# Performance work log

Measured on AMD Instinct MI355X. Metric: run time of the kernel, lower is better.

The kernel has to match this reference:

```python
import jax, jax.numpy as jnp
import numpy as np

B, S, D_IN, D_OUT = 4, 4096, 1024, 64

def setup_inputs() -> dict:
    key = jax.random.key(0)
    ks = jax.random.split(key, 7)
    return {
        "x":  jax.random.normal(ks[0], (B, S, D_IN), dtype=jnp.float32),
        "Wq": jax.random.normal(ks[1], (D_IN, D_OUT), dtype=jnp.float32) * 0.02,
        "bq": jax.random.normal(ks[2], (D_OUT,), dtype=jnp.float32) * 0.02,
        "Wk": jax.random.normal(ks[3], (D_IN, D_OUT), dtype=jnp.float32) * 0.02,
        "bk": jax.random.normal(ks[4], (D_OUT,), dtype=jnp.float32) * 0.02,
        "Wv": jax.random.normal(ks[5], (D_IN, D_OUT), dtype=jnp.float32) * 0.02,
        "bv": jax.random.normal(ks[6], (D_OUT,), dtype=jnp.float32) * 0.02,
    }

def reference(x, Wq, bq, Wk, bk, Wv, bv):
    # x: [B, S, d_in]
    seq = x.shape[1]
    q = x @ Wq + bq            # [B, S, d_out]
    k = x @ Wk + bk
    v = x @ Wv + bv
    scores = jnp.einsum("bqd,bkd->bqk", q, k)          # [B, S, S]
    causal = jnp.triu(jnp.ones((seq, seq), dtype=bool), k=1)
    scores = jnp.where(causal[None, :, :], -jnp.inf, scores)
    # NOTE: original code scales by sqrt(token_len), not sqrt(d_out) (d_k = keys.shape[1])
    scale = jnp.sqrt(jnp.asarray(seq, dtype=scores.dtype))
    attn = jax.nn.softmax(scores / scale, axis=-1)      # [B, S, S]
    # dropout in the original is applied but its result is discarded -> no-op
    return jnp.einsum("bqk,bkd->bqd", attn, v)          # [B, S, d_out]
```

## Files before the change

kernel.cpp:

```cpp
#include <hip/hip_runtime.h>
#include <math.h>

#define B 4
#define S 4096
#define DIN 1024
#define DOUT 64
#define BS (B * S)

typedef __bf16 bf16;
typedef __bf16 bf16x4 __attribute__((ext_vector_type(4)));
typedef __bf16 bf16x8 __attribute__((ext_vector_type(8)));
typedef float f32x4 __attribute__((ext_vector_type(4)));

#define QSCALE 0.022542110013890053f

#define QS_OFF 0
#define KF_OFF (2u * 1024 * 1024)
#define VF_OFF (4u * 1024 * 1024)
#define WP_OFF (6u * 1024 * 1024)
#define OP_OFF (7u * 1024 * 1024)
#define LP_OFF (23u * 1024 * 1024)

__global__ __launch_bounds__(256) void wpack_kernel(
    const float* __restrict__ Wq, const float* __restrict__ Wk,
    const float* __restrict__ Wv, bf16* __restrict__ wp) {
  const int t = blockIdx.x * 256 + threadIdx.x;
  const int m = t >> 16;
  const int r = t & 65535;
  const int k = r >> 6;
  const int n64 = r & 63;
  const float* W = (m == 0) ? Wq : (m == 1) ? Wk : Wv;
  const float v = W[r];
  const int n = m * 64 + n64;
  const int nt = n >> 4;
  const int lane = ((k >> 3) & 3) * 16 + (n & 15);
  const int idx = ((nt * 32 + (k >> 5)) * 64 + lane) * 8 + (k & 7);
  wp[idx] = (bf16)v;
}

__global__ __launch_bounds__(256) void qkv_mfma_kernel(
    const float* __restrict__ x, const float* __restrict__ bq,
    const float* __restrict__ bk, const float* __restrict__ bv,
    const bf16* __restrict__ wp, bf16* __restrict__ Qs,
    bf16* __restrict__ KF, bf16* __restrict__ VF) {
  __shared__ __align__(16) bf16 xt[32][520];

  const int tid = threadIdx.x;
  const int wid = tid >> 6;
  const int lane = tid & 63;
  const int l15 = lane & 15;
  const int quad = lane >> 4;
  const int blk = blockIdx.x;

  const bf16x8* wp8 = (const bf16x8*)wp;

  f32x4 acc[3][2];
#pragma unroll
  for (int j = 0; j < 3; ++j)
#pragma unroll
    for (int st = 0; st < 2; ++st) acc[j][st] = (f32x4)(0.f);

  for (int ph = 0; ph < 2; ++ph) {
    if (ph) __syncthreads();
    {
      float4 v[16];
#pragma unroll
      for (int i = 0; i < 16; ++i) {
        const int ch = i * 256 + tid;
        const int row = ch >> 7;
        const int col4 = ch & 127;
        v[i] = *(const float4*)(x + (size_t)(blk * 32 + row) * DIN + ph * 512 +
                                col4 * 4);
      }
#pragma unroll
      for (int i = 0; i < 16; ++i) {
        const int ch = i * 256 + tid;
        const int row = ch >> 7;
        const int col4 = ch & 127;
        bf16x4 c;
        c[0] = (bf16)v[i].x; c[1] = (bf16)v[i].y;
        c[2] = (bf16)v[i].z; c[3] = (bf16)v[i].w;
        *(bf16x4*)&xt[row][col4 * 4] = c;
      }
    }
    __syncthreads();

#pragma unroll 4
    for (int kc = 0; kc < 16; ++kc) {
      bf16x8 bfr[3];
#pragma unroll
      for (int j = 0; j < 3; ++j)
        bfr[j] = wp8[((wid * 3 + j) * 32 + ph * 16 + kc) * 64 + lane];
      const bf16x8 a0 = *(const bf16x8*)&xt[l15][quad * 8 + kc * 32];
      const bf16x8 a1 = *(const bf16x8*)&xt[16 + l15][quad * 8 + kc * 32];
#pragma unroll
      for (int j = 0; j < 3; ++j) {
        acc[j][0] = __builtin_amdgcn_mfma_f32_16x16x32_bf16(a0, bfr[j], acc[j][0], 0, 0, 0);
        acc[j][1] = __builtin_amdgcn_mfma_f32_16x16x32_bf16(a1, bfr[j], acc[j][1], 0, 0, 0);
      }
    }
  }

#pragma unroll
  for (int j = 0; j < 3; ++j) {
    const int nt = wid * 3 + j;
    const int sel = nt >> 2;
    const int c = (nt & 3) * 16 + l15;
    const float bias = ((sel == 0) ? bq : (sel == 1) ? bk : bv)[c];
#pragma unroll
    for (int st = 0; st < 2; ++st) {
      const int row0 = blk * 32 + st * 16 + quad * 4;
      if (sel == 0) {
#pragma unroll
        for (int r = 0; r < 4; ++r)
          Qs[(size_t)(row0 + r) * DOUT + c] =
              (bf16)((acc[j][st][r] + bias) * QSCALE);
      } else if (sel == 1) {
        const size_t kb =
            ((size_t)(((row0 >> 6) * 4 + ((row0 >> 4) & 3)) * 2 + (c >> 5)) * 64 +
             ((c >> 3) & 3) * 16 + quad * 4) * 8 + (c & 7);
#pragma unroll
        for (int r = 0; r < 4; ++r)
          KF[kb + r * 8] = (bf16)(acc[j][st][r] + bias);
      } else {
        const size_t vb =
            ((size_t)(((row0 >> 6) * 2 + ((row0 >> 5) & 1)) * 4 + (c >> 4)) * 64 +
             (c & 15) + 16 * ((row0 >> 3) & 3)) * 8 + (row0 & 7);
        bf16x4 vv;
#pragma unroll
        for (int r = 0; r < 4; ++r) vv[r] = (bf16)(acc[j][st][r] + bias);
        *(bf16x4*)(VF + vb) = vv;
      }
    }
  }
}

__global__ __launch_bounds__(256) void attn_mfma_kernel(
    const bf16* __restrict__ Qs, const bf16* __restrict__ KFp,
    const bf16* __restrict__ VFp, bf16* __restrict__ Oh,
    float* __restrict__ lh) {
  __shared__ __align__(16) bf16 pw[4][32][72];

  const int tid = threadIdx.x;
  const int wid = tid >> 6;
  const int lane = tid & 63;
  const int l15 = lane & 15;
  const int quad = lane >> 4;
  const int b = blockIdx.x & 3;
  const int half = (blockIdx.x >> 2) & 1;
  const int s32 = 127 - (blockIdx.x >> 3);
  const int ntiles = (s32 >> 1) + 1;
  const int e = half * 4 + wid;
  const int t0 = (e * ntiles) >> 3;
  const int t1 = ((e + 1) * ntiles) >> 3;

  const bf16x8* KF8 = (const bf16x8*)KFp;
  const bf16x8* VF8 = (const bf16x8*)VFp;
  const int tb0 = b * 64;

  const bf16* Qb = Qs + ((size_t)b * S + s32 * 32) * DOUT;
  bf16x8 qf[2][2];
#pragma unroll
  for (int st = 0; st < 2; ++st)
#pragma unroll
    for (int k = 0; k < 2; ++k)
      qf[st][k] =
          *(const bf16x8*)(Qb + (st * 16 + l15) * DOUT + k * 32 + quad * 8);

  f32x4 o[2][4];
#pragma unroll
  for (int st = 0; st < 2; ++st)
#pragma unroll
    for (int i = 0; i < 4; ++i) o[st][i] = (f32x4)(0.f);
  f32x4 lsum[2] = {(f32x4)(0.f), (f32x4)(0.f)};

  for (int t = t0; t < t1; ++t) {
    const int tb = tb0 + t;
    bf16x8 kf[8], vf[8];
#pragma unroll
    for (int nt = 0; nt < 4; ++nt)
#pragma unroll
      for (int c = 0; c < 2; ++c)
        kf[nt * 2 + c] = KF8[(size_t)((tb * 4 + nt) * 2 + c) * 64 + lane];
#pragma unroll
    for (int c = 0; c < 2; ++c)
#pragma unroll
      for (int ntd = 0; ntd < 4; ++ntd)
        vf[c * 4 + ntd] = VF8[(size_t)((tb * 2 + c) * 4 + ntd) * 64 + lane];

    f32x4 s[2][4];
#pragma unroll
    for (int st = 0; st < 2; ++st)
#pragma unroll
      for (int nt = 0; nt < 4; ++nt) {
        s[st][nt] = __builtin_amdgcn_mfma_f32_16x16x32_bf16(
            qf[st][0], kf[nt * 2 + 0], (f32x4)(0.f), 0, 0, 0);
        s[st][nt] = __builtin_amdgcn_mfma_f32_16x16x32_bf16(
            qf[st][1], kf[nt * 2 + 1], s[st][nt], 0, 0, 0);
      }

    if (t == ntiles - 1) {
#pragma unroll
      for (int st = 0; st < 2; ++st)
#pragma unroll
        for (int nt = 0; nt < 4; ++nt) {
          const int key = t * 64 + nt * 16 + l15;
#pragma unroll
          for (int r = 0; r < 4; ++r) {
            const int qrow = s32 * 32 + st * 16 + quad * 4 + r;
            const float p = (key <= qrow) ? exp2f(fminf(s[st][nt][r], 44.f)) : 0.f;
            lsum[st][r] += p;
            pw[wid][st * 16 + quad * 4 + r][nt * 16 + l15] = (bf16)p;
          }
        }
    } else {
#pragma unroll
      for (int st = 0; st < 2; ++st)
#pragma unroll
        for (int nt = 0; nt < 4; ++nt)
#pragma unroll
          for (int r = 0; r < 4; ++r) {
            const float p = exp2f(fminf(s[st][nt][r], 44.f));
            lsum[st][r] += p;
            pw[wid][st * 16 + quad * 4 + r][nt * 16 + l15] = (bf16)p;
          }
    }

#pragma unroll
    for (int st = 0; st < 2; ++st) {
      const bf16x8 pf0 = *(const bf16x8*)&pw[wid][st * 16 + l15][quad * 8];
      const bf16x8 pf1 = *(const bf16x8*)&pw[wid][st * 16 + l15][32 + quad * 8];
#pragma unroll
      for (int ntd = 0; ntd < 4; ++ntd) {
        o[st][ntd] = __builtin_amdgcn_mfma_f32_16x16x32_bf16(
            pf0, vf[0 * 4 + ntd], o[st][ntd], 0, 0, 0);
        o[st][ntd] = __builtin_amdgcn_mfma_f32_16x16x32_bf16(
            pf1, vf[1 * 4 + ntd], o[st][ntd], 0, 0, 0);
      }
    }
  }

#pragma unroll
  for (int m = 1; m < 16; m <<= 1)
#pragma unroll
    for (int st = 0; st < 2; ++st)
#pragma unroll
      for (int r = 0; r < 4; ++r) lsum[st][r] += __shfl_xor(lsum[st][r], m, 64);

  const int slot = (b * 128 + s32) * 8 + e;
  if (l15 == 0) {
#pragma unroll
    for (int st = 0; st < 2; ++st)
#pragma unroll
      for (int r = 0; r < 4; ++r)
        lh[slot * 32 + st * 16 + quad * 4 + r] = lsum[st][r];
  }
#pragma unroll
  for (int st = 0; st < 2; ++st)
#pragma unroll
    for (int ntd = 0; ntd < 4; ++ntd)
#pragma unroll
      for (int r = 0; r < 4; ++r)
        Oh[(size_t)slot * 2048 + (st * 16 + quad * 4 + r) * 64 + ntd * 16 + l15] =
            (bf16)o[st][ntd][r];
}

__global__ __launch_bounds__(256) void combine_kernel(
    const bf16* __restrict__ Oh, const float* __restrict__ lh,
    float* __restrict__ out) {
  const int gid = blockIdx.x * 256 + threadIdx.x;
  const int token = gid >> 4;
  const int d4 = (gid & 15) * 4;
  const int b = token >> 12;
  const int s = token & 4095;
  const int s32 = s >> 5;
  const int qq = s & 31;
  const int slot0 = (b * 128 + s32) * 8;
  f32x4 acc = (f32x4)(0.f);
  float l = 0.f;
#pragma unroll
  for (int q = 0; q < 8; ++q) {
    const bf16x4 ov =
        *(const bf16x4*)(Oh + (size_t)(slot0 + q) * 2048 + qq * 64 + d4);
#pragma unroll
    for (int i = 0; i < 4; ++i) acc[i] += (float)ov[i];
    l += lh[(slot0 + q) * 32 + qq];
  }
  ((f32x4*)out)[gid] = acc * (1.f / l);
}

extern "C" void kernel_launch(void* const* d_in, const int* in_sizes, int n_in,
                              void* d_out, int out_size, void* d_ws,
                              size_t ws_size, hipStream_t stream) {
  const float* x  = (const float*)d_in[0];
  const float* Wq = (const float*)d_in[1];
  const float* bq = (const float*)d_in[2];
  const float* Wk = (const float*)d_in[3];
  const float* bk = (const float*)d_in[4];
  const float* Wv = (const float*)d_in[5];
  const float* bv = (const float*)d_in[6];
  float* out = (float*)d_out;

  char* ws = (char*)d_ws;
  bf16* Qs = (bf16*)(ws + QS_OFF);
  bf16* KF = (bf16*)(ws + KF_OFF);
  bf16* VF = (bf16*)(ws + VF_OFF);
  bf16* wp = (bf16*)(ws + WP_OFF);
  bf16* Oh = (bf16*)(ws + OP_OFF);
  float* lh = (float*)(ws + LP_OFF);

  wpack_kernel<<<768, 256, 0, stream>>>(Wq, Wk, Wv, wp);
  qkv_mfma_kernel<<<512, 256, 0, stream>>>(x, bq, bk, bv, wp, Qs, KF, VF);
  attn_mfma_kernel<<<1024, 256, 0, stream>>>(Qs, KF, VF, Oh, lh);
  combine_kernel<<<1024, 256, 0, stream>>>(Oh, lh, out);
}
```

Baseline: 150.4 us.

## Double waves in QKV projection and prefetch second x half during first MMA phase

The QKV projection block goes from 256 to 512 threads, with each wave handling one 16-row subtile instead of two, so there are more waves to hide latency. The global load of the second half of x is issued before the first-phase MFMA loop and written to shared memory afterwards, overlapping load latency with compute. The trade-off is that every wave now reloads the same weight fragments, doubling weight traffic per block, and the prefetched values occupy extra registers.

```diff
diff --git a/kernel.cpp b/kernel.cpp
--- a/kernel.cpp
+++ b/kernel.cpp
@@ -38,7 +38,7 @@
   wp[idx] = (bf16)v;
 }
 
-__global__ __launch_bounds__(256) void qkv_mfma_kernel(
+__global__ __launch_bounds__(512, 4) void qkv_mfma_kernel(
     const float* __restrict__ x, const float* __restrict__ bq,
     const float* __restrict__ bk, const float* __restrict__ bv,
     const bf16* __restrict__ wp, bf16* __restrict__ Qs,
@@ -50,87 +50,104 @@
   const int lane = tid & 63;
   const int l15 = lane & 15;
   const int quad = lane >> 4;
+  const int st = wid >> 2;
+  const int w4 = wid & 3;
   const int blk = blockIdx.x;
 
   const bf16x8* wp8 = (const bf16x8*)wp;
 
-  f32x4 acc[3][2];
-#pragma unroll
-  for (int j = 0; j < 3; ++j)
-#pragma unroll
-    for (int st = 0; st < 2; ++st) acc[j][st] = (f32x4)(0.f);
-
-  for (int ph = 0; ph < 2; ++ph) {
-    if (ph) __syncthreads();
-    {
-      float4 v[16];
-#pragma unroll
-      for (int i = 0; i < 16; ++i) {
-        const int ch = i * 256 + tid;
-        const int row = ch >> 7;
-        const int col4 = ch & 127;
-        v[i] = *(const float4*)(x + (size_t)(blk * 32 + row) * DIN + ph * 512 +
-                                col4 * 4);
-      }
-#pragma unroll
-      for (int i = 0; i < 16; ++i) {
-        const int ch = i * 256 + tid;
-        const int row = ch >> 7;
-        const int col4 = ch & 127;
-        bf16x4 c;
-        c[0] = (bf16)v[i].x; c[1] = (bf16)v[i].y;
-        c[2] = (bf16)v[i].z; c[3] = (bf16)v[i].w;
-        *(bf16x4*)&xt[row][col4 * 4] = c;
-      }
-    }
-    __syncthreads();
+  f32x4 acc[3];
+#pragma unroll
+  for (int j = 0; j < 3; ++j) acc[j] = (f32x4)(0.f);
+
+  float4 v[8];
+
+#pragma unroll
+  for (int i = 0; i < 8; ++i) {
+    const int ch = i * 512 + tid;
+    v[i] = *(const float4*)(x + (size_t)(blk * 32 + (ch >> 7)) * DIN +
+                            (ch & 127) * 4);
+  }
+#pragma unroll
+  for (int i = 0; i < 8; ++i) {
+    const int ch = i * 512 + tid;
+    bf16x4 c4;
+    c4[0] = (bf16)v[i].x; c4[1] = (bf16)v[i].y;
+    c4[2] = (bf16)v[i].z; c4[3] = (bf16)v[i].w;
+    *(bf16x4*)&xt[ch >> 7][(ch & 127) * 4] = c4;
+  }
+  __syncthreads();
+
+#pragma unroll
+  for (int i = 0; i < 8; ++i) {
+    const int ch = i * 512 + tid;
+    v[i] = *(const float4*)(x + (size_t)(blk * 32 + (ch >> 7)) * DIN + 512 +
+                            (ch & 127) * 4);
+  }
+  __builtin_amdgcn_sched_barrier(0);
 
 #pragma unroll 4
-    for (int kc = 0; kc < 16; ++kc) {
-      bf16x8 bfr[3];
-#pragma unroll
-      for (int j = 0; j < 3; ++j)
-        bfr[j] = wp8[((wid * 3 + j) * 32 + ph * 16 + kc) * 64 + lane];
-      const bf16x8 a0 = *(const bf16x8*)&xt[l15][quad * 8 + kc * 32];
-      const bf16x8 a1 = *(const bf16x8*)&xt[16 + l15][quad * 8 + kc * 32];
-#pragma unroll
-      for (int j = 0; j < 3; ++j) {
-        acc[j][0] = __builtin_amdgcn_mfma_f32_16x16x32_bf16(a0, bfr[j], acc[j][0], 0, 0, 0);
-        acc[j][1] = __builtin_amdgcn_mfma_f32_16x16x32_bf16(a1, bfr[j], acc[j][1], 0, 0, 0);
-      }
-    }
+  for (int kc = 0; kc < 16; ++kc) {
+    bf16x8 bfr[3];
+#pragma unroll
+    for (int j = 0; j < 3; ++j)
+      bfr[j] = wp8[((w4 * 3 + j) * 32 + kc) * 64 + lane];
+    const bf16x8 a = *(const bf16x8*)&xt[st * 16 + l15][quad * 8 + kc * 32];
+#pragma unroll
+    for (int j = 0; j < 3; ++j)
+      acc[j] = __builtin_amdgcn_mfma_f32_16x16x32_bf16(a, bfr[j], acc[j], 0, 0, 0);
+  }
+  __syncthreads();
+
+#pragma unroll
+  for (int i = 0; i < 8; ++i) {
+    const int ch = i * 512 + tid;
+    bf16x4 c4;
+    c4[0] = (bf16)v[i].x; c4[1] = (bf16)v[i].y;
+    c4[2] = (bf16)v[i].z; c4[3] = (bf16)v[i].w;
+    *(bf16x4*)&xt[ch >> 7][(ch & 127) * 4] = c4;
+  }
+  __syncthreads();
+
+#pragma unroll 4
+  for (int kc = 0; kc < 16; ++kc) {
+    bf16x8 bfr[3];
+#pragma unroll
+    for (int j = 0; j < 3; ++j)
+      bfr[j] = wp8[((w4 * 3 + j) * 32 + 16 + kc) * 64 + lane];
+    const bf16x8 a = *(const bf16x8*)&xt[st * 16 + l15][quad * 8 + kc * 32];
+#pragma unroll
+    for (int j = 0; j < 3; ++j)
+      acc[j] = __builtin_amdgcn_mfma_f32_16x16x32_bf16(a, bfr[j], acc[j], 0, 0, 0);
   }
 
 #pragma unroll
   for (int j = 0; j < 3; ++j) {
-    const int nt = wid * 3 + j;
+    const int nt = w4 * 3 + j;
     const int sel = nt >> 2;
     const int c = (nt & 3) * 16 + l15;
     const float bias = ((sel == 0) ? bq : (sel == 1) ? bk : bv)[c];
-#pragma unroll
-    for (int st = 0; st < 2; ++st) {
-      const int row0 = blk * 32 + st * 16 + quad * 4;
-      if (sel == 0) {
-#pragma unroll
-        for (int r = 0; r < 4; ++r)
-          Qs[(size_t)(row0 + r) * DOUT + c] =
-              (bf16)((acc[j][st][r] + bias) * QSCALE);
-      } else if (sel == 1) {
-        const size_t kb =
-            ((size_t)(((row0 >> 6) * 4 + ((row0 >> 4) & 3)) * 2 + (c >> 5)) * 64 +
-             ((c >> 3) & 3) * 16 + quad * 4) * 8 + (c & 7);
-#pragma unroll
-        for (int r = 0; r < 4; ++r)
-          KF[kb + r * 8] = (bf16)(acc[j][st][r] + bias);
-      } else {
-        const size_t vb =
-            ((size_t)(((row0 >> 6) * 2 + ((row0 >> 5) & 1)) * 4 + (c >> 4)) * 64 +
-             (c & 15) + 16 * ((row0 >> 3) & 3)) * 8 + (row0 & 7);
-        bf16x4 vv;
-#pragma unroll
-        for (int r = 0; r < 4; ++r) vv[r] = (bf16)(acc[j][st][r] + bias);
-        *(bf16x4*)(VF + vb) = vv;
-      }
+    const int row0 = blk * 32 + st * 16 + quad * 4;
+    if (sel == 0) {
+#pragma unroll
+      for (int r = 0; r < 4; ++r)
+        Qs[(size_t)(row0 + r) * DOUT + c] =
+            (bf16)((acc[j][r] + bias) * QSCALE);
+    } else if (sel == 1) {
+      const size_t kb =
+          ((size_t)(((row0 >> 6) * 4 + ((row0 >> 4) & 3)) * 2 + (c >> 5)) * 64 +
+           ((c >> 3) & 3) * 16 + quad * 4) * 8 + (c & 7);
+#pragma unroll
+      for (int r = 0; r < 4; ++r)
+        KF[kb + r * 8] = (bf16)(acc[j][r] + bias);
+    } else {
+      const size_t vb =
+          ((size_t)(((row0 >> 6) * 2 + ((row0 >> 5) & 1)) * 4 + (c >> 4)) * 64 +
+           (c & 15) + 16 * ((row0 >> 3) & 3)) * 8 + (row0 & 7);
+      bf16x4 vv;
+#pragma unroll
+      for (int r = 0; r < 4; ++r) vv[r] = (bf16)(acc[j][r] + bias);
+      *(bf16x4*)(VF + vb) = vv;
     }
   }
 }
@@ -310,7 +327,7 @@
   float* lh = (float*)(ws + LP_OFF);
 
   wpack_kernel<<<768, 256, 0, stream>>>(Wq, Wk, Wv, wp);
-  qkv_mfma_kernel<<<512, 256, 0, stream>>>(x, bq, bk, bv, wp, Qs, KF, VF);
+  qkv_mfma_kernel<<<512, 512, 0, stream>>>(x, bq, bk, bv, wp, Qs, KF, VF);
   attn_mfma_kernel<<<1024, 256, 0, stream>>>(Qs, KF, VF, Oh, lh);
   combine_kernel<<<1024, 256, 0, stream>>>(Oh, lh, out);
 }
```

Measured after the change: 151.7 us. Within noise of the previous version (+0.9%).

## Fuse QKV projection and attention into one persistent kernel with per-batch counters

Applied to the files above, without the earlier changes.

Merges the QKV projection and attention kernels into a single 512-block launch. Each block first computes its projection tile, then signals a per-batch atomic counter, and then runs two attention work units after spinning until every projection block of that batch has finished. The counters are zeroed in the weight-pack kernel. This removes a kernel launch and lets attention for one batch start while other batches are still projecting. In exchange it relies on all 512 blocks being co-resident (launch bounds request 2 blocks per CU) to avoid deadlock, and adds spin-wait and fence overhead.

```diff
diff --git a/kernel.cpp b/kernel.cpp
--- a/kernel.cpp
+++ b/kernel.cpp
@@ -20,10 +20,13 @@
 #define WP_OFF (6u * 1024 * 1024)
 #define OP_OFF (7u * 1024 * 1024)
 #define LP_OFF (23u * 1024 * 1024)
+#define CNT_OFF (30u * 1024 * 1024)
 
 __global__ __launch_bounds__(256) void wpack_kernel(
     const float* __restrict__ Wq, const float* __restrict__ Wk,
-    const float* __restrict__ Wv, bf16* __restrict__ wp) {
+    const float* __restrict__ Wv, bf16* __restrict__ wp,
+    int* __restrict__ cnt) {
+  if (blockIdx.x == 0 && threadIdx.x < 4) cnt[threadIdx.x] = 0;
   const int t = blockIdx.x * 256 + threadIdx.x;
   const int m = t >> 16;
   const int r = t & 65535;
@@ -38,231 +41,248 @@
   wp[idx] = (bf16)v;
 }
 
-__global__ __launch_bounds__(256) void qkv_mfma_kernel(
+__global__ __launch_bounds__(256, 2) void qkvattn_kernel(
     const float* __restrict__ x, const float* __restrict__ bq,
     const float* __restrict__ bk, const float* __restrict__ bv,
     const bf16* __restrict__ wp, bf16* __restrict__ Qs,
-    bf16* __restrict__ KF, bf16* __restrict__ VF) {
-  __shared__ __align__(16) bf16 xt[32][520];
+    bf16* __restrict__ KF, bf16* __restrict__ VF, bf16* __restrict__ Oh,
+    float* __restrict__ lh, int* __restrict__ cnt) {
+  __shared__ __align__(16) char smem[33280];
 
   const int tid = threadIdx.x;
+  const int bid = blockIdx.x;
   const int wid = tid >> 6;
   const int lane = tid & 63;
   const int l15 = lane & 15;
   const int quad = lane >> 4;
-  const int blk = blockIdx.x;
-
-  const bf16x8* wp8 = (const bf16x8*)wp;
-
-  f32x4 acc[3][2];
-#pragma unroll
-  for (int j = 0; j < 3; ++j)
-#pragma unroll
-    for (int st = 0; st < 2; ++st) acc[j][st] = (f32x4)(0.f);
-
-  for (int ph = 0; ph < 2; ++ph) {
-    if (ph) __syncthreads();
-    {
-      float4 v[16];
-#pragma unroll
-      for (int i = 0; i < 16; ++i) {
-        const int ch = i * 256 + tid;
-        const int row = ch >> 7;
-        const int col4 = ch & 127;
-        v[i] = *(const float4*)(x + (size_t)(blk * 32 + row) * DIN + ph * 512 +
-                                col4 * 4);
-      }
-#pragma unroll
-      for (int i = 0; i < 16; ++i) {
-        const int ch = i * 256 + tid;
-        const int row = ch >> 7;
-        const int col4 = ch & 127;
-        bf16x4 c;
-        c[0] = (bf16)v[i].x; c[1] = (bf16)v[i].y;
-        c[2] = (bf16)v[i].z; c[3] = (bf16)v[i].w;
-        *(bf16x4*)&xt[row][col4 * 4] = c;
-      }
+
+  {
+    bf16(*xt)[520] = (bf16(*)[520])smem;
+    const int blk = bid;
+    const bf16x8* wp8 = (const bf16x8*)wp;
+
+    f32x4 acc[3][2];
+#pragma unroll
+    for (int j = 0; j < 3; ++j)
+#pragma unroll
+      for (int st = 0; st < 2; ++st) acc[j][st] = (f32x4)(0.f);
+
+    for (int ph = 0; ph < 2; ++ph) {
+      if (ph) __syncthreads();
+      {
+        float4 v[16];
+#pragma unroll
+        for (int i = 0; i < 16; ++i) {
+          const int ch = i * 256 + tid;
+          const int row = ch >> 7;
+          const int col4 = ch & 127;
+          v[i] = *(const float4*)(x + (size_t)(blk * 32 + row) * DIN +
+                                  ph * 512 + col4 * 4);
+        }
+#pragma unroll
+        for (int i = 0; i < 16; ++i) {
+          const int ch = i * 256 + tid;
+          const int row = ch >> 7;
+          const int col4 = ch & 127;
+          bf16x4 c;
+          c[0] = (bf16)v[i].x; c[1] = (bf16)v[i].y;
+          c[2] = (bf16)v[i].z; c[3] = (bf16)v[i].w;
+          *(bf16x4*)&xt[row][col4 * 4] = c;
+        }
+      }
+      __syncthreads();
+
+#pragma unroll 4
+      for (int kc = 0; kc < 16; ++kc) {
+        bf16x8 bfr[3];
+#pragma unroll
+        for (int j = 0; j < 3; ++j)
+          bfr[j] = wp8[((wid * 3 + j) * 32 + ph * 16 + kc) * 64 + lane];
+        const bf16x8 a0 = *(const bf16x8*)&xt[l15][quad * 8 + kc * 32];
+        const bf16x8 a1 = *(const bf16x8*)&xt[16 + l15][quad * 8 + kc * 32];
+#pragma unroll
+        for (int j = 0; j < 3; ++j) {
+          acc[j][0] = __builtin_amdgcn_mfma_f32_16x16x32_bf16(a0, bfr[j],
+                                                              acc[j][0], 0, 0, 0);
+          acc[j][1] = __builtin_amdgcn_mfma_f32_16x16x32_bf16(a1, bfr[j],
+                                                              acc[j][1], 0, 0, 0);
+        }
+      }
+    }
+
+#pragma unroll
+    for (int j = 0; j < 3; ++j) {
+      const int nt = wid * 3 + j;
+      const int sel = nt >> 2;
+      const int c = (nt & 3) * 16 + l15;
+      const float bias = ((sel == 0) ? bq : (sel == 1) ? bk : bv)[c];
+#pragma unroll
+      for (int st = 0; st < 2; ++st) {
+        const int row0 = blk * 32 + st * 16 + quad * 4;
+        if (sel == 0) {
+#pragma unroll
+          for (int r = 0; r < 4; ++r)
+            Qs[(size_t)(row0 + r) * DOUT + c] =
+                (bf16)((acc[j][st][r] + bias) * QSCALE);
+        } else if (sel == 1) {
+          const size_t kb =
+              ((size_t)(((row0 >> 6) * 4 + ((row0 >> 4) & 3)) * 2 + (c >> 5)) *
+                   64 + ((c >> 3) & 3) * 16 + quad * 4) * 8 + (c & 7);
+#pragma unroll
+          for (int r = 0; r < 4; ++r)
+            KF[kb + r * 8] = (bf16)(acc[j][st][r] + bias);
+        } else {
+          const size_t vb =
+              ((size_t)(((row0 >> 6) * 2 + ((row0 >> 5) & 1)) * 4 + (c >> 4)) *
+                   64 + (c & 15) + 16 * ((row0 >> 3) & 3)) * 8 + (row0 & 7);
+          bf16x4 vv;
+#pragma unroll
+          for (int r = 0; r < 4; ++r) vv[r] = (bf16)(acc[j][st][r] + bias);
+          *(bf16x4*)(VF + vb) = vv;
+        }
+      }
+    }
+  }
+
+  __threadfence();
+  __syncthreads();
+  if (tid == 0)
+    __hip_atomic_fetch_add(&cnt[bid >> 7], 1, __ATOMIC_RELEASE,
+                           __HIP_MEMORY_SCOPE_AGENT);
+
+  bf16(*pw)[32][72] = (bf16(*)[32][72])smem;
+  const bf16x8* KF8 = (const bf16x8*)KF;
+  const bf16x8* VF8 = (const bf16x8*)VF;
+
+#pragma unroll 1
+  for (int pass = 0; pass < 2; ++pass) {
+    const int u = pass ? (512 + (bid ^ 128)) : bid;
+    const int b = u >> 8;
+    const int rr = u & 255;
+    const int s32 = 127 - (rr >> 1);
+    const int half = rr & 1;
+    const int ntiles = (s32 >> 1) + 1;
+    const int e = half * 4 + wid;
+    const int t0 = (e * ntiles) >> 3;
+    const int t1 = ((e + 1) * ntiles) >> 3;
+    const int tb0 = b * 64;
+
+    if (tid == 0) {
+      while (__hip_atomic_load(&cnt[b], __ATOMIC_ACQUIRE,
+                               __HIP_MEMORY_SCOPE_AGENT) < 128)
+        __builtin_amdgcn_s_sleep(8);
     }
     __syncthreads();
 
-#pragma unroll 4
-    for (int kc = 0; kc < 16; ++kc) {
-      bf16x8 bfr[3];
-#pragma unroll
-      for (int j = 0; j < 3; ++j)
-        bfr[j] = wp8[((wid * 3 + j) * 32 + ph * 16 + kc) * 64 + lane];
-      const bf16x8 a0 = *(const bf16x8*)&xt[l15][quad * 8 + kc * 32];
-      const bf16x8 a1 = *(const bf16x8*)&xt[16 + l15][quad * 8 + kc * 32];
-#pragma unroll
-      for (int j = 0; j < 3; ++j) {
-        acc[j][0] = __builtin_amdgcn_mfma_f32_16x16x32_bf16(a0, bfr[j], acc[j][0], 0, 0, 0);
-        acc[j][1] = __builtin_amdgcn_mfma_f32_16x16x32_bf16(a1, bfr[j], acc[j][1], 0, 0, 0);
-      }
-    }
+    const bf16* Qb = Qs + ((size_t)b * S + s32 * 32) * DOUT;
+    bf16x8 qf[2][2];
+#pragma unroll
+    for (int st = 0; st < 2; ++st)
+#pragma unroll
+      for (int k = 0; k < 2; ++k)
+        qf[st][k] =
+            *(const bf16x8*)(Qb + (st * 16 + l15) * DOUT + k * 32 + quad * 8);
+
+    f32x4 o[2][4];
+#pragma unroll
+    for (int st = 0; st < 2; ++st)
+#pragma unroll
+      for (int i = 0; i < 4; ++i) o[st][i] = (f32x4)(0.f);
+    f32x4 lsum[2] = {(f32x4)(0.f), (f32x4)(0.f)};
+
+    for (int t = t0; t < t1; ++t) {
+      const int tb = tb0 + t;
+      bf16x8 kf[8], vf[8];
+#pragma unroll
+      for (int nt = 0; nt < 4; ++nt)
+#pragma unroll
+        for (int c = 0; c < 2; ++c)
+          kf[nt * 2 + c] = KF8[(size_t)((tb * 4 + nt) * 2 + c) * 64 + lane];
+#pragma unroll
+      for (int c = 0; c < 2; ++c)
+#pragma unroll
+        for (int ntd = 0; ntd < 4; ++ntd)
+          vf[c * 4 + ntd] = VF8[(size_t)((tb * 2 + c) * 4 + ntd) * 64 + lane];
+
+      f32x4 s[2][4];
+#pragma unroll
+      for (int st = 0; st < 2; ++st)
+#pragma unroll
+        for (int nt = 0; nt < 4; ++nt) {
+          s[st][nt] = __builtin_amdgcn_mfma_f32_16x16x32_bf16(
+              qf[st][0], kf[nt * 2 + 0], (f32x4)(0.f), 0, 0, 0);
+          s[st][nt] = __builtin_amdgcn_mfma_f32_16x16x32_bf16(
+              qf[st][1], kf[nt * 2 + 1], s[st][nt], 0, 0, 0);
+        }
+
+      if (t == ntiles - 1) {
+#pragma unroll
+        for (int st = 0; st < 2; ++st)
+#pragma unroll
+          for (int nt = 0; nt < 4; ++nt) {
+            const int key = t * 64 + nt * 16 + l15;
+#pragma unroll
+            for (int r = 0; r < 4; ++r) {
+              const int qrow = s32 * 32 + st * 16 + quad * 4 + r;
+              const float p =
+                  (key <= qrow) ? exp2f(fminf(s[st][nt][r], 44.f)) : 0.f;
+              lsum[st][r] += p;
+              pw[wid][st * 16 + quad * 4 + r][nt * 16 + l15] = (bf16)p;
+            }
+          }
+      } else {
+#pragma unroll
+        for (int st = 0; st < 2; ++st)
+#pragma unroll
+          for (int nt = 0; nt < 4; ++nt)
+#pragma unroll
+            for (int r = 0; r < 4; ++r) {
+              const float p = exp2f(fminf(s[st][nt][r], 44.f));
+              lsum[st][r] += p;
+              pw[wid][st * 16 + quad * 4 + r][nt * 16 + l15] = (bf16)p;
+            }
+      }
+
+#pragma unroll
+      for (int st = 0; st < 2; ++st) {
+        const bf16x8 pf0 = *(const bf16x8*)&pw[wid][st * 16 + l15][quad * 8];
+        const bf16x8 pf1 =
+            *(const bf16x8*)&pw[wid][st * 16 + l15][32 + quad * 8];
+#pragma unroll
+        for (int ntd = 0; ntd < 4; ++ntd) {
+          o[st][ntd] = __builtin_amdgcn_mfma_f32_16x16x32_bf16(
+              pf0, vf[0 * 4 + ntd], o[st][ntd], 0, 0, 0);
+          o[st][ntd] = __builtin_amdgcn_mfma_f32_16x16x32_bf16(
+              pf1, vf[1 * 4 + ntd], o[st][ntd], 0, 0, 0);
+        }
+      }
+    }
+
+#pragma unroll
+    for (int m = 1; m < 16; m <<= 1)
+#pragma unroll
+      for (int st = 0; st < 2; ++st)
+#pragma unroll
+        for (int r = 0; r < 4; ++r)
+          lsum[st][r] += __shfl_xor(lsum[st][r], m, 64);
+
+    const int slot = (b * 128 + s32) * 8 + e;
+    if (l15 == 0) {
+#pragma unroll
+      for (int st = 0; st < 2; ++st)
+#pragma unroll
+        for (int r = 0; r < 4; ++r)
+          lh[slot * 32 + st * 16 + quad * 4 + r] = lsum[st][r];
+    }
+#pragma unroll
+    for (int st = 0; st < 2; ++st)
+#pragma unroll
+      for (int ntd = 0; ntd < 4; ++ntd)
+#pragma unroll
+        for (int r = 0; r < 4; ++r)
+          Oh[(size_t)slot * 2048 + (st * 16 + quad * 4 + r) * 64 + ntd * 16 +
+             l15] = (bf16)o[st][ntd][r];
   }
-
-#pragma unroll
-  for (int j = 0; j < 3; ++j) {
-    const int nt = wid * 3 + j;
-    const int sel = nt >> 2;
-    const int c = (nt & 3) * 16 + l15;
-    const float bias = ((sel == 0) ? bq : (sel == 1) ? bk : bv)[c];
-#pragma unroll
-    for (int st = 0; st < 2; ++st) {
-      const int row0 = blk * 32 + st * 16 + quad * 4;
-      if (sel == 0) {
-#pragma unroll
-        for (int r = 0; r < 4; ++r)
-          Qs[(size_t)(row0 + r) * DOUT + c] =
-              (bf16)((acc[j][st][r] + bias) * QSCALE);
-      } else if (sel == 1) {
-        const size_t kb =
-            ((size_t)(((row0 >> 6) * 4 + ((row0 >> 4) & 3)) * 2 + (c >> 5)) * 64 +
-             ((c >> 3) & 3) * 16 + quad * 4) * 8 + (c & 7);
-#pragma unroll
-        for (int r = 0; r < 4; ++r)
-          KF[kb + r * 8] = (bf16)(acc[j][st][r] + bias);
-      } else {
-        const size_t vb =
-            ((size_t)(((row0 >> 6) * 2 + ((row0 >> 5) & 1)) * 4 + (c >> 4)) * 64 +
-             (c & 15) + 16 * ((row0 >> 3) & 3)) * 8 + (row0 & 7);
-        bf16x4 vv;
-#pragma unroll
-        for (int r = 0; r < 4; ++r) vv[r] = (bf16)(acc[j][st][r] + bias);
-        *(bf16x4*)(VF + vb) = vv;
-      }
-    }
-  }
-}
-
-__global__ __launch_bounds__(256) void attn_mfma_kernel(
-    const bf16* __restrict__ Qs, const bf16* __restrict__ KFp,
-    const bf16* __restrict__ VFp, bf16* __restrict__ Oh,
-    float* __restrict__ lh) {
-  __shared__ __align__(16) bf16 pw[4][32][72];
-
-  const int tid = threadIdx.x;
-  const int wid = tid >> 6;
-  const int lane = tid & 63;
-  const int l15 = lane & 15;
-  const int quad = lane >> 4;
-  const int b = blockIdx.x & 3;
-  const int half = (blockIdx.x >> 2) & 1;
-  const int s32 = 127 - (blockIdx.x >> 3);
-  const int ntiles = (s32 >> 1) + 1;
-  const int e = half * 4 + wid;
-  const int t0 = (e * ntiles) >> 3;
-  const int t1 = ((e + 1) * ntiles) >> 3;
-
-  const bf16x8* KF8 = (const bf16x8*)KFp;
-  const bf16x8* VF8 = (const bf16x8*)VFp;
-  const int tb0 = b * 64;
-
-  const bf16* Qb = Qs + ((size_t)b * S + s32 * 32) * DOUT;
-  bf16x8 qf[2][2];
-#pragma unroll
-  for (int st = 0; st < 2; ++st)
-#pragma unroll
-    for (int k = 0; k < 2; ++k)
-      qf[st][k] =
-          *(const bf16x8*)(Qb + (st * 16 + l15) * DOUT + k * 32 + quad * 8);
-
-  f32x4 o[2][4];
-#pragma unroll
-  for (int st = 0; st < 2; ++st)
-#pragma unroll
-    for (int i = 0; i < 4; ++i) o[st][i] = (f32x4)(0.f);
-  f32x4 lsum[2] = {(f32x4)(0.f), (f32x4)(0.f)};
-
-  for (int t = t0; t < t1; ++t) {
-    const int tb = tb0 + t;
-    bf16x8 kf[8], vf[8];
-#pragma unroll
-    for (int nt = 0; nt < 4; ++nt)
-#pragma unroll
-      for (int c = 0; c < 2; ++c)
-        kf[nt * 2 + c] = KF8[(size_t)((tb * 4 + nt) * 2 + c) * 64 + lane];
-#pragma unroll
-    for (int c = 0; c < 2; ++c)
-#pragma unroll
-      for (int ntd = 0; ntd < 4; ++ntd)
-        vf[c * 4 + ntd] = VF8[(size_t)((tb * 2 + c) * 4 + ntd) * 64 + lane];
-
-    f32x4 s[2][4];
-#pragma unroll
-    for (int st = 0; st < 2; ++st)
-#pragma unroll
-      for (int nt = 0; nt < 4; ++nt) {
-        s[st][nt] = __builtin_amdgcn_mfma_f32_16x16x32_bf16(
-            qf[st][0], kf[nt * 2 + 0], (f32x4)(0.f), 0, 0, 0);
-        s[st][nt] = __builtin_amdgcn_mfma_f32_16x16x32_bf16(
-            qf[st][1], kf[nt * 2 + 1], s[st][nt], 0, 0, 0);
-      }
-
-    if (t == ntiles - 1) {
-#pragma unroll
-      for (int st = 0; st < 2; ++st)
-#pragma unroll
-        for (int nt = 0; nt < 4; ++nt) {
-          const int key = t * 64 + nt * 16 + l15;
-#pragma unroll
-          for (int r = 0; r < 4; ++r) {
-            const int qrow = s32 * 32 + st * 16 + quad * 4 + r;
-            const float p = (key <= qrow) ? exp2f(fminf(s[st][nt][r], 44.f)) : 0.f;
-            lsum[st][r] += p;
-            pw[wid][st * 16 + quad * 4 + r][nt * 16 + l15] = (bf16)p;
-          }
-        }
-    } else {
-#pragma unroll
-      for (int st = 0; st < 2; ++st)
-#pragma unroll
-        for (int nt = 0; nt < 4; ++nt)
-#pragma unroll
-          for (int r = 0; r < 4; ++r) {
-            const float p = exp2f(fminf(s[st][nt][r], 44.f));
-            lsum[st][r] += p;
-            pw[wid][st * 16 + quad * 4 + r][nt * 16 + l15] = (bf16)p;
-          }
-    }
-
-#pragma unroll
-    for (int st = 0; st < 2; ++st) {
-      const bf16x8 pf0 = *(const bf16x8*)&pw[wid][st * 16 + l15][quad * 8];
-      const bf16x8 pf1 = *(const bf16x8*)&pw[wid][st * 16 + l15][32 + quad * 8];
-#pragma unroll
-      for (int ntd = 0; ntd < 4; ++ntd) {
-        o[st][ntd] = __builtin_amdgcn_mfma_f32_16x16x32_bf16(
-            pf0, vf[0 * 4 + ntd], o[st][ntd], 0, 0, 0);
-        o[st][ntd] = __builtin_amdgcn_mfma_f32_16x16x32_bf16(
-            pf1, vf[1 * 4 + ntd], o[st][ntd], 0, 0, 0);
-      }
-    }
-  }
-
-#pragma unroll
-  for (int m = 1; m < 16; m <<= 1)
-#pragma unroll
-    for (int st = 0; st < 2; ++st)
-#pragma unroll
-      for (int r = 0; r < 4; ++r) lsum[st][r] += __shfl_xor(lsum[st][r], m, 64);
-
-  const int slot = (b * 128 + s32) * 8 + e;
-  if (l15 == 0) {
-#pragma unroll
-    for (int st = 0; st < 2; ++st)
-#pragma unroll
-      for (int r = 0; r < 4; ++r)
-        lh[slot * 32 + st * 16 + quad * 4 + r] = lsum[st][r];
-  }
-#pragma unroll
-  for (int st = 0; st < 2; ++st)
-#pragma unroll
-    for (int ntd = 0; ntd < 4; ++ntd)
-#pragma unroll
-      for (int r = 0; r < 4; ++r)
-        Oh[(size_t)slot * 2048 + (st * 16 + quad * 4 + r) * 64 + ntd * 16 + l15] =
-            (bf16)o[st][ntd][r];
 }
 
 __global__ __launch_bounds__(256) void combine_kernel(
@@ -308,9 +328,10 @@
   bf16* wp = (bf16*)(ws + WP_OFF);
   bf16* Oh = (bf16*)(ws + OP_OFF);
   float* lh = (float*)(ws + LP_OFF);
-
-  wpack_kernel<<<768, 256, 0, stream>>>(Wq, Wk, Wv, wp);
-  qkv_mfma_kernel<<<512, 256, 0, stream>>>(x, bq, bk, bv, wp, Qs, KF, VF);
-  attn_mfma_kernel<<<1024, 256, 0, stream>>>(Qs, KF, VF, Oh, lh);
+  int* cnt = (int*)(ws + CNT_OFF);
+
+  wpack_kernel<<<768, 256, 0, stream>>>(Wq, Wk, Wv, wp, cnt);
+  qkvattn_kernel<<<512, 256, 0, stream>>>(x, bq, bk, bv, wp, Qs, KF, VF, Oh,
+                                          lh, cnt);
   combine_kernel<<<1024, 256, 0, stream>>>(Oh, lh, out);
 }
```

Result: slower. 235.1 us (+56.3%).
